# Kernel tuning notes

Measured on AMD Instinct MI355X. Metric: run time of the kernel, lower is better.

## Reference

```python
import jax, jax.numpy as jnp
import numpy as np

EMBED_DIM = 1024
NUM_HEADS = 16
HEAD_DIM = EMBED_DIM // NUM_HEADS


def setup_inputs() -> dict:
    key = jax.random.key(0)
    ks = jax.random.split(key, 5)
    s = 1.0 / np.sqrt(EMBED_DIM)
    x = jax.random.normal(ks[0], (2, 2048, EMBED_DIM), dtype=jnp.float32)
    Wq = jax.random.normal(ks[1], (EMBED_DIM, EMBED_DIM), dtype=jnp.float32) * s
    Wk = jax.random.normal(ks[2], (EMBED_DIM, EMBED_DIM), dtype=jnp.float32) * s
    Wv = jax.random.normal(ks[3], (EMBED_DIM, EMBED_DIM), dtype=jnp.float32) * s
    Wo = jax.random.normal(ks[4], (EMBED_DIM, EMBED_DIM), dtype=jnp.float32) * s
    z = jnp.zeros((EMBED_DIM,), dtype=jnp.float32)
    return {"x": x, "Wq": Wq, "bq": z, "Wk": Wk, "bk": z, "Wv": Wv, "bv": z, "Wo": Wo, "bo": z}


def reference(x, Wq, bq, Wk, bk, Wv, bv, Wo, bo):
    B, S, E = x.shape
    H, D = NUM_HEADS, HEAD_DIM
    # projections; weights stored as [in, out] so y = x @ W + b
    q = (x @ Wq + bq).reshape(B, S, H, D).transpose(0, 2, 1, 3)  # [B,H,S,D]
    k = (x @ Wk + bk).reshape(B, S, H, D).transpose(0, 2, 1, 3)
    v = (x @ Wv + bv).reshape(B, S, H, D).transpose(0, 2, 1, 3)
    scores = jnp.einsum('bhqd,bhkd->bhqk', q, k) / jnp.sqrt(jnp.float32(D))
    attn = jax.nn.softmax(scores, axis=-1)
    out = jnp.einsum('bhqk,bhkd->bhqd', attn, v)  # [B,H,S,D]
    out = out.transpose(0, 2, 1, 3).reshape(B, S, E)
    return out @ Wo + bo
```

## Files before the change

kernel.cpp:

```cpp
#include <hip/hip_runtime.h>
#include <cstdint>
#include <cstddef>

typedef __attribute__((ext_vector_type(8))) short bf16x8;
typedef __attribute__((ext_vector_type(4))) float f32x4;
typedef __attribute__((ext_vector_type(16))) float f32x16;
typedef __attribute__((ext_vector_type(4))) unsigned int u32x4;
typedef __attribute__((ext_vector_type(2))) unsigned int u32x2;

__device__ __forceinline__ unsigned short f2bf(float f) {
    union { float f; unsigned int u; } c; c.f = f;
    unsigned int r = c.u + 0x7FFFu + ((c.u >> 16) & 1u);
    return (unsigned short)(r >> 16);
}
__device__ __forceinline__ unsigned int pack2bf(float a, float b) {
    return (unsigned int)f2bf(a) | ((unsigned int)f2bf(b) << 16);
}
__device__ __forceinline__ unsigned int cvtpk(float lo, float hi) {
    unsigned int r;
    asm("v_cvt_pk_bf16_f32 %0, %1, %2" : "=v"(r) : "v"(lo), "v"(hi));
    return r;
}
__device__ __forceinline__ void gload16(const void* g, void* l) {
    __builtin_amdgcn_global_load_lds((const __attribute__((address_space(1))) void*)g,
                                     (__attribute__((address_space(3))) void*)l, 16, 0, 0);
}
__device__ __forceinline__ float tmax16(const f32x16& v) {
    float a0 = fmaxf(v[0], v[1]),   a1 = fmaxf(v[2], v[3]);
    float a2 = fmaxf(v[4], v[5]),   a3 = fmaxf(v[6], v[7]);
    float a4 = fmaxf(v[8], v[9]),   a5 = fmaxf(v[10], v[11]);
    float a6 = fmaxf(v[12], v[13]), a7 = fmaxf(v[14], v[15]);
    float b0 = fmaxf(a0, a1), b1 = fmaxf(a2, a3);
    float b2 = fmaxf(a4, a5), b3 = fmaxf(a6, a7);
    return fmaxf(fmaxf(b0, b1), fmaxf(b2, b3));
}
__device__ __forceinline__ float tsum16(const float* p) {
    float a0 = p[0] + p[1],   a1 = p[2] + p[3];
    float a2 = p[4] + p[5],   a3 = p[6] + p[7];
    float a4 = p[8] + p[9],   a5 = p[10] + p[11];
    float a6 = p[12] + p[13], a7 = p[14] + p[15];
    float b0 = a0 + a1, b1 = a2 + a3, b2 = a4 + a5, b3 = a6 + a7;
    return (b0 + b1) + (b2 + b3);
}

__global__ __launch_bounds__(256) void cvt_kernel(const float* __restrict__ x,
    const float* __restrict__ w0, const float* __restrict__ w1,
    const float* __restrict__ w2, const float* __restrict__ w3,
    unsigned short* __restrict__ xdst, unsigned short* __restrict__ wdst) {
    __shared__ unsigned short sm[64][68];
    const int bid = blockIdx.x;
    const int tid = threadIdx.x;
    if (bid >= 1024) {
        int e = ((bid - 1024) * 256 + tid) * 8;
        const float4* s4 = reinterpret_cast<const float4*>(x + e);
        float4 a = s4[0], b = s4[1];
        u32x4 o;
        o.x = pack2bf(a.x, a.y); o.y = pack2bf(a.z, a.w);
        o.z = pack2bf(b.x, b.y); o.w = pack2bf(b.z, b.w);
        *reinterpret_cast<u32x4*>(xdst + e) = o;
        return;
    }
    int z = bid >> 8, xb = bid & 255;
    const float* src = (z == 0) ? w0 : (z == 1) ? w1 : (z == 2) ? w2 : w3;
    unsigned short* dst = wdst + (size_t)z * 1048576;
    int n0 = (xb & 15) * 64;
    int k0 = (xb >> 4) * 64;
    #pragma unroll
    for (int i = 0; i < 4; i++) {
        int e = i * 1024 + tid * 4;
        int r = e >> 6, c = e & 63;
        float4 v = *reinterpret_cast<const float4*>(src + (size_t)(k0 + r) * 1024 + n0 + c);
        u32x2 p; p.x = pack2bf(v.x, v.y); p.y = pack2bf(v.z, v.w);
        *reinterpret_cast<u32x2*>(&sm[r][c]) = p;
    }
    __syncthreads();
    #pragma unroll
    for (int i = 0; i < 4; i++) {
        int e = i * 1024 + tid * 4;
        int n = e >> 6, kk = e & 63;
        u32x2 p;
        p.x = (unsigned)sm[kk][n]     | ((unsigned)sm[kk + 1][n] << 16);
        p.y = (unsigned)sm[kk + 2][n] | ((unsigned)sm[kk + 3][n] << 16);
        *reinterpret_cast<u32x2*>(dst + (size_t)(n0 + n) * 1024 + k0 + kk) = p;
    }
}

__device__ __forceinline__ void gemm128_main(
    const unsigned short* __restrict__ A, const unsigned short* __restrict__ Wt,
    int m0, int n0, int tid,
    unsigned short* Asm, unsigned short* Bsm,
    f32x4 acc[4][4])
{
    const int lane = tid & 63;
    const int w = tid >> 6;
    const int wm = w >> 1, wn = w & 1;
    const int lr = lane & 15, lg = lane >> 4;
    for (int k0 = 0; k0 < 1024; k0 += 64) {
        __syncthreads();
        #pragma unroll
        for (int i = 0; i < 4; i++) {
            int L = (i * 4 + w) * 64 + lane;
            int r = L >> 3, cs = L & 7;
            int c = cs ^ (r & 7);
            gload16(A  + (size_t)(m0 + r) * 1024 + k0 + c * 8, Asm + (i * 4 + w) * 512);
            gload16(Wt + (size_t)(n0 + r) * 1024 + k0 + c * 8, Bsm + (i * 4 + w) * 512);
        }
        __syncthreads();
        #pragma unroll
        for (int ks = 0; ks < 2; ks++) {
            bf16x8 af[4], bfr[4];
            #pragma unroll
            for (int t = 0; t < 4; t++) {
                int Ra = wm * 64 + t * 16 + lr;
                af[t]  = *reinterpret_cast<const bf16x8*>(Asm + Ra * 64 + ((ks * 4 + lg) ^ (Ra & 7)) * 8);
                int Rb = wn * 64 + t * 16 + lr;
                bfr[t] = *reinterpret_cast<const bf16x8*>(Bsm + Rb * 64 + ((ks * 4 + lg) ^ (Rb & 7)) * 8);
            }
            #pragma unroll
            for (int mt = 0; mt < 4; mt++) {
                #pragma unroll
                for (int nt = 0; nt < 4; nt++)
                    acc[mt][nt] = __builtin_amdgcn_mfma_f32_16x16x32_bf16(af[mt], bfr[nt], acc[mt][nt], 0, 0, 0);
            }
        }
    }
}

__global__ __launch_bounds__(256) void gemm_qkv_kernel(
    const unsigned short* __restrict__ A, const unsigned short* __restrict__ WtBase,
    const float* __restrict__ bq, const float* __restrict__ bk, const float* __restrict__ bv,
    unsigned short* __restrict__ Qo, unsigned short* __restrict__ Ko, unsigned short* __restrict__ Vto)
{
    __shared__ unsigned short Asm[8192];
    __shared__ unsigned short Bsm[8192];
    const int bid = blockIdx.x;
    const int wg = (bid & 7) * 96 + (bid >> 3);
    const int z = wg >> 8;
    const int rem = wg & 255;
    const int m0 = (rem >> 3) * 128, n0 = (rem & 7) * 128;
    const unsigned short* Wt = WtBase + (size_t)z * 1048576;
    const float* bias = (z == 0) ? bq : (z == 1) ? bk : bv;
    const int tid = threadIdx.x, lane = tid & 63, w = tid >> 6;
    const int wm = w >> 1, wn = w & 1, lr = lane & 15, lg = lane >> 4;
    f32x4 acc[4][4];
    f32x4 zero4 = {0.f, 0.f, 0.f, 0.f};
    #pragma unroll
    for (int i = 0; i < 4; i++)
        #pragma unroll
        for (int j = 0; j < 4; j++) acc[i][j] = zero4;
    gemm128_main(A, Wt, m0, n0, tid, Asm, Bsm, acc);

    const float qs = 0.125f * 1.44269504088896341f;
    #pragma unroll
    for (int mt = 0; mt < 4; mt++) {
        #pragma unroll
        for (int nt = 0; nt < 4; nt++) {
            int gn = n0 + wn * 64 + nt * 16 + lr;
            int h = gn >> 6, d = gn & 63;
            int rb = m0 + wm * 64 + mt * 16 + lg * 4;
            int b_ = rb >> 11, s = rb & 2047;
            float bv_ = bias[gn];
            if (z == 2) {
                u32x2 p;
                p.x = pack2bf(acc[mt][nt][0] + bv_, acc[mt][nt][1] + bv_);
                p.y = pack2bf(acc[mt][nt][2] + bv_, acc[mt][nt][3] + bv_);
                *reinterpret_cast<u32x2*>(Vto + ((size_t)(b_ * 16 + h) * 64 + d) * 2048 + s) = p;
            } else {
                unsigned short* dst = (z == 0) ? Qo : Ko;
                float sc_ = (z == 0) ? qs : 1.0f;
                #pragma unroll
                for (int r = 0; r < 4; r++)
                    dst[((size_t)(b_ * 16 + h) * 2048 + (s + r)) * 64 + d] = f2bf((acc[mt][nt][r] + bv_) * sc_);
            }
        }
    }
}

__global__ __launch_bounds__(256, 2) void attn_kernel(
    const unsigned short* __restrict__ Qg,
    const unsigned short* __restrict__ Kg,
    const unsigned short* __restrict__ Vtg,
    unsigned short* __restrict__ Og)
{
    __shared__ unsigned short Ksm[128][72];
    __shared__ unsigned short Vsm[64][136];

    const int tid = threadIdx.x, lane = tid & 63, w = tid >> 6;
    const int l31 = lane & 31, L = lane >> 5;
    const int bh = blockIdx.y, q0 = blockIdx.x * 128;
    const size_t kvbase = (size_t)bh * (2048 * 64);
    const size_t vtbase = (size_t)bh * (64 * 2048);

    {
        u32x4 qr[4];
        #pragma unroll
        for (int i = 0; i < 4; i++) {
            int ck = i * 256 + tid; int r = ck >> 3, c = (ck & 7) * 8;
            qr[i] = *reinterpret_cast<const u32x4*>(Qg + kvbase + (size_t)(q0 + r) * 64 + c);
        }
        #pragma unroll
        for (int i = 0; i < 4; i++) {
            int ck = i * 256 + tid; int r = ck >> 3, c = (ck & 7) * 8;
            *reinterpret_cast<u32x4*>(&Ksm[r][c]) = qr[i];
        }
    }
    __syncthreads();
    bf16x8 qf[4];
    #pragma unroll
    for (int ds = 0; ds < 4; ds++)
        qf[ds] = *reinterpret_cast<const bf16x8*>(&Ksm[w * 32 + l31][ds * 16 + L * 8]);
    __syncthreads();

    f32x16 oacc[2];
    #pragma unroll
    for (int dt = 0; dt < 2; dt++)
        #pragma unroll
        for (int j = 0; j < 16; j++) oacc[dt][j] = 0.f;
    float m_run = -3.0e38f, l_run = 0.f;

    u32x4 kreg[4], vreg[4];
#define LOAD_TILE(KV0)                                                                      \
    _Pragma("unroll")                                                                       \
    for (int i = 0; i < 4; i++) {                                                           \
        int ck = i * 256 + tid; int r = ck >> 3, c = (ck & 7) * 8;                          \
        kreg[i] = *reinterpret_cast<const u32x4*>(Kg + kvbase + (size_t)((KV0) + r) * 64 + c); \
        int dv = ck >> 4, cv = (ck & 15) * 8;                                               \
        vreg[i] = *reinterpret_cast<const u32x4*>(Vtg + vtbase + (size_t)dv * 2048 + (KV0) + cv); \
    }

    LOAD_TILE(0)
    for (int kt = 0; kt < 16; kt++) {
        #pragma unroll
        for (int i = 0; i < 4; i++) {
            int ck = i * 256 + tid; int r = ck >> 3, c = (ck & 7) * 8;
            *reinterpret_cast<u32x4*>(&Ksm[r][c]) = kreg[i];
            int dv = ck >> 4, cv = (ck & 15) * 8;
            *reinterpret_cast<u32x4*>(&Vsm[dv][cv]) = vreg[i];
        }
        __syncthreads();
        int kvn = (kt < 15) ? (kt + 1) * 128 : 0;
        LOAD_TILE(kvn)

        f32x16 sc[4];
        #pragma unroll
        for (int nt = 0; nt < 4; nt++) {
            #pragma unroll
            for (int j = 0; j < 16; j++) sc[nt][j] = 0.f;
            #pragma unroll
            for (int ds = 0; ds < 4; ds++) {
                bf16x8 kf = *reinterpret_cast<const bf16x8*>(&Ksm[nt * 32 + l31][ds * 16 + L * 8]);
                sc[nt] = __builtin_amdgcn_mfma_f32_32x32x16_bf16(kf, qf[ds], sc[nt], 0, 0, 0);
            }
        }

        float pmax = fmaxf(fmaxf(tmax16(sc[0]), tmax16(sc[1])),
                           fmaxf(tmax16(sc[2]), tmax16(sc[3])));
        pmax = fmaxf(pmax, __shfl_xor(pmax, 32));

        if (__any(pmax - m_run > 8.0f)) {
            float mnew = fmaxf(m_run, pmax);
            float f = __builtin_amdgcn_exp2f(m_run - mnew);
            l_run *= f;
            #pragma unroll
            for (int dt = 0; dt < 2; dt++)
                #pragma unroll
                for (int j = 0; j < 16; j++) oacc[dt][j] *= f;
            m_run = mnew;
        }

        float psum = 0.f;
        unsigned pdw[4][4][2];
        #pragma unroll
        for (int nt = 0; nt < 4; nt++) {
            float p[16];
            #pragma unroll
            for (int j = 0; j < 16; j++)
                p[j] = __builtin_amdgcn_exp2f(sc[nt][j] - m_run);
            psum += tsum16(p);
            #pragma unroll
            for (int a = 0; a < 4; a++) {
                pdw[nt][a][0] = cvtpk(p[4 * a + 0], p[4 * a + 1]);
                pdw[nt][a][1] = cvtpk(p[4 * a + 2], p[4 * a + 3]);
            }
        }
        psum += __shfl_xor(psum, 32);
        l_run += psum;

        bf16x8 pfr[8];
        #pragma unroll
        for (int kt2 = 0; kt2 < 8; kt2++) {
            const int nt = kt2 >> 1, b2 = (kt2 & 1) * 2;
            unsigned own0  = L ? pdw[nt][b2 + 1][0] : pdw[nt][b2][0];
            unsigned own1  = L ? pdw[nt][b2 + 1][1] : pdw[nt][b2][1];
            unsigned send0 = L ? pdw[nt][b2][0]     : pdw[nt][b2 + 1][0];
            unsigned send1 = L ? pdw[nt][b2][1]     : pdw[nt][b2 + 1][1];
            unsigned recv0 = (unsigned)__shfl_xor((int)send0, 32);
            unsigned recv1 = (unsigned)__shfl_xor((int)send1, 32);
            u32x4 pf4;
            pf4.x = L ? recv0 : own0;
            pf4.y = L ? recv1 : own1;
            pf4.z = L ? own0  : recv0;
            pf4.w = L ? own1  : recv1;
            pfr[kt2] = *reinterpret_cast<bf16x8*>(&pf4);
        }
        #pragma unroll
        for (int kt2 = 0; kt2 < 8; kt2++) {
            #pragma unroll
            for (int dt = 0; dt < 2; dt++) {
                bf16x8 vf = *reinterpret_cast<const bf16x8*>(&Vsm[dt * 32 + l31][kt2 * 16 + L * 8]);
                oacc[dt] = __builtin_amdgcn_mfma_f32_32x32x16_bf16(vf, pfr[kt2], oacc[dt], 0, 0, 0);
            }
        }
        __syncthreads();
    }
#undef LOAD_TILE

    float inv = 1.0f / l_run;
    const int b_ = bh >> 4, h = bh & 15;
    const int s = q0 + w * 32 + l31;
    unsigned short* orow = Og + ((size_t)b_ * 2048 + s) * 1024 + h * 64;
    #pragma unroll
    for (int dt = 0; dt < 2; dt++) {
        #pragma unroll
        for (int g = 0; g < 4; g++) {
            u32x2 pp;
            pp.x = cvtpk(oacc[dt][4 * g + 0] * inv, oacc[dt][4 * g + 1] * inv);
            pp.y = cvtpk(oacc[dt][4 * g + 2] * inv, oacc[dt][4 * g + 3] * inv);
            *reinterpret_cast<u32x2*>(orow + dt * 32 + g * 8 + 4 * L) = pp;
        }
    }
}

__global__ __launch_bounds__(256) void gemm_out_kernel(
    const unsigned short* __restrict__ A, const unsigned short* __restrict__ Wt,
    const float* __restrict__ bias, float* __restrict__ out)
{
    __shared__ unsigned short Asm[8192];
    __shared__ unsigned short Bsm[8192];
    const int bid = blockIdx.x;
    const int wg = (bid & 7) * 32 + (bid >> 3);
    const int m0 = (wg >> 3) * 128, n0 = (wg & 7) * 128;
    const int tid = threadIdx.x, lane = tid & 63, w = tid >> 6;
    const int wm = w >> 1, wn = w & 1, lr = lane & 15, lg = lane >> 4;
    f32x4 acc[4][4];
    f32x4 zero4 = {0.f, 0.f, 0.f, 0.f};
    #pragma unroll
    for (int i = 0; i < 4; i++)
        #pragma unroll
        for (int j = 0; j < 4; j++) acc[i][j] = zero4;
    gemm128_main(A, Wt, m0, n0, tid, Asm, Bsm, acc);
    #pragma unroll
    for (int mt = 0; mt < 4; mt++) {
        #pragma unroll
        for (int nt = 0; nt < 4; nt++) {
            int gn = n0 + wn * 64 + nt * 16 + lr;
            float bv_ = bias[gn];
            int rb = m0 + wm * 64 + mt * 16 + lg * 4;
            #pragma unroll
            for (int r = 0; r < 4; r++)
                out[(size_t)(rb + r) * 1024 + gn] = acc[mt][nt][r] + bv_;
        }
    }
}

extern "C" void kernel_launch(void* const* d_in, const int* in_sizes, int n_in,
                              void* d_out, int out_size, void* d_ws, size_t ws_size,
                              hipStream_t stream) {
    const float* x  = (const float*)d_in[0];
    const float* Wq = (const float*)d_in[1];
    const float* bq = (const float*)d_in[2];
    const float* Wk = (const float*)d_in[3];
    const float* bk = (const float*)d_in[4];
    const float* Wv = (const float*)d_in[5];
    const float* bv = (const float*)d_in[6];
    const float* Wo = (const float*)d_in[7];
    const float* bo = (const float*)d_in[8];
    float* out = (float*)d_out;

    if (ws_size < (size_t)25165824 * 2) return;
    unsigned short* ws  = (unsigned short*)d_ws;
    unsigned short* xbf = ws;
    unsigned short* wt  = ws + 4194304;
    unsigned short* Qb  = ws + 8388608;
    unsigned short* Kb  = ws + 12582912;
    unsigned short* Vtb = ws + 16777216;
    unsigned short* Ob  = ws + 20971520;

    cvt_kernel<<<3072, 256, 0, stream>>>(x, Wq, Wk, Wv, Wo, xbf, wt);
    gemm_qkv_kernel<<<768, 256, 0, stream>>>(xbf, wt, bq, bk, bv, Qb, Kb, Vtb);
    attn_kernel<<<dim3(16, 32), 256, 0, stream>>>(Qb, Kb, Vtb, Ob);
    gemm_out_kernel<<<256, 256, 0, stream>>>(Ob, wt + 3 * 1048576, bo, out);
}
```

Baseline: 132.4 us.

## Permute K rows in shared memory so P fragments need no cross-lane shuffle

K tile rows are stored with an XOR-based row permutation, so the S=K·Q^T accumulator comes out with kv indices arranged such that each lane's P values already match the B-operand layout of the PV MFMA. This removes the eight pairs of __shfl_xor exchanges and selects per tile that previously rebuilt the P fragments. The first MFMA of each score tile also accumulates into a zero vector instead of zeroing sc first. Correctness now relies on the row permutation exactly matching the MFMA output layout, and the V shared-memory layout is left unchanged.

```diff
diff --git a/kernel.cpp b/kernel.cpp
--- a/kernel.cpp
+++ b/kernel.cpp
@@ -218,6 +218,10 @@
         for (int j = 0; j < 16; j++) oacc[dt][j] = 0.f;
     float m_run = -3.0e38f, l_run = 0.f;
 
+    f32x16 z16;
+    #pragma unroll
+    for (int j = 0; j < 16; j++) z16[j] = 0.f;
+
     u32x4 kreg[4], vreg[4];
 #define LOAD_TILE(KV0)                                                                      \
     _Pragma("unroll")                                                                       \
@@ -233,7 +237,8 @@
         #pragma unroll
         for (int i = 0; i < 4; i++) {
             int ck = i * 256 + tid; int r = ck >> 3, c = (ck & 7) * 8;
-            *reinterpret_cast<u32x4*>(&Ksm[r][c]) = kreg[i];
+            int rp = r ^ (((((r >> 2) ^ (r >> 3)) & 1)) * 12);
+            *reinterpret_cast<u32x4*>(&Ksm[rp][c]) = kreg[i];
             int dv = ck >> 4, cv = (ck & 15) * 8;
             *reinterpret_cast<u32x4*>(&Vsm[dv][cv]) = vreg[i];
         }
@@ -244,10 +249,12 @@
         f32x16 sc[4];
         #pragma unroll
         for (int nt = 0; nt < 4; nt++) {
-            #pragma unroll
-            for (int j = 0; j < 16; j++) sc[nt][j] = 0.f;
-            #pragma unroll
-            for (int ds = 0; ds < 4; ds++) {
+            {
+                bf16x8 kf = *reinterpret_cast<const bf16x8*>(&Ksm[nt * 32 + l31][L * 8]);
+                sc[nt] = __builtin_amdgcn_mfma_f32_32x32x16_bf16(kf, qf[0], z16, 0, 0, 0);
+            }
+            #pragma unroll
+            for (int ds = 1; ds < 4; ds++) {
                 bf16x8 kf = *reinterpret_cast<const bf16x8*>(&Ksm[nt * 32 + l31][ds * 16 + L * 8]);
                 sc[nt] = __builtin_amdgcn_mfma_f32_32x32x16_bf16(kf, qf[ds], sc[nt], 0, 0, 0);
             }
@@ -286,29 +293,19 @@
         psum += __shfl_xor(psum, 32);
         l_run += psum;
 
-        bf16x8 pfr[8];
         #pragma unroll
         for (int kt2 = 0; kt2 < 8; kt2++) {
-            const int nt = kt2 >> 1, b2 = (kt2 & 1) * 2;
-            unsigned own0  = L ? pdw[nt][b2 + 1][0] : pdw[nt][b2][0];
-            unsigned own1  = L ? pdw[nt][b2 + 1][1] : pdw[nt][b2][1];
-            unsigned send0 = L ? pdw[nt][b2][0]     : pdw[nt][b2 + 1][0];
-            unsigned send1 = L ? pdw[nt][b2][1]     : pdw[nt][b2 + 1][1];
-            unsigned recv0 = (unsigned)__shfl_xor((int)send0, 32);
-            unsigned recv1 = (unsigned)__shfl_xor((int)send1, 32);
+            const int nt = kt2 >> 1, c2 = (kt2 & 1) * 2;
             u32x4 pf4;
-            pf4.x = L ? recv0 : own0;
-            pf4.y = L ? recv1 : own1;
-            pf4.z = L ? own0  : recv0;
-            pf4.w = L ? own1  : recv1;
-            pfr[kt2] = *reinterpret_cast<bf16x8*>(&pf4);
-        }
-        #pragma unroll
-        for (int kt2 = 0; kt2 < 8; kt2++) {
+            pf4.x = pdw[nt][c2][0];
+            pf4.y = pdw[nt][c2][1];
+            pf4.z = pdw[nt][c2 + 1][0];
+            pf4.w = pdw[nt][c2 + 1][1];
+            bf16x8 pfr = *reinterpret_cast<bf16x8*>(&pf4);
             #pragma unroll
             for (int dt = 0; dt < 2; dt++) {
                 bf16x8 vf = *reinterpret_cast<const bf16x8*>(&Vsm[dt * 32 + l31][kt2 * 16 + L * 8]);
-                oacc[dt] = __builtin_amdgcn_mfma_f32_32x32x16_bf16(vf, pfr[kt2], oacc[dt], 0, 0, 0);
+                oacc[dt] = __builtin_amdgcn_mfma_f32_32x32x16_bf16(vf, pfr, oacc[dt], 0, 0, 0);
             }
         }
         __syncthreads();
```

New measurement: 129.1 us. 1.02x faster.
